# Optimization experiments

Measured on AMD Instinct MI355X. Metric: run time of the kernel, lower is better.

## Reference

```python
import jax, jax.numpy as jnp
import numpy as np

K = 8              # kernel_size
C_IN = 3           # input_channels
HID = 256          # hidden_state_size
MID = 256          # mid_layer_size
N_MAIN = 4         # num_main_layers
N_CLS = 1000       # num_classes
N_PIX = K * K      # num_pixel_values
IN_VEC = 2 + 1 + N_PIX * C_IN + HID   # 451
OUT_VEC = 2 + 1 + HID                 # 259
B, H, W = 128, 256, 256


def _lin_init(k, fan_in, fan_out):
    kw, kb = jax.random.split(k)
    bound = 1.0 / np.sqrt(fan_in)
    w = jax.random.uniform(kw, (fan_in, fan_out), jnp.float32, -bound, bound)
    b = jax.random.uniform(kb, (fan_out,), jnp.float32, -bound, bound)
    return w, b


def setup_inputs() -> dict:
    key = jax.random.key(0)
    ks = jax.random.split(key, 16)
    image = jax.random.normal(ks[0], (B, C_IN, H, W), jnp.float32)
    locations = jax.random.uniform(ks[1], (B, 2), jnp.float32)
    scales = jax.random.uniform(ks[2], (B, 1), jnp.float32)
    hidden_state = jax.random.normal(ks[3], (B, HID), jnp.float32)
    w0, b0 = _lin_init(ks[4], IN_VEC, MID)
    rws, rbs = [], []
    for i in range(N_MAIN):
        w, b = _lin_init(jax.random.fold_in(ks[5], i), MID, MID)
        rws.append(w); rbs.append(b)
    rw = jnp.stack(rws); rb = jnp.stack(rbs)          # [4,MID,MID], [4,MID]
    wf, bf = _lin_init(ks[6], MID, OUT_VEC)
    cw0, cb0 = _lin_init(ks[7], HID, MID)
    crw, crb = _lin_init(ks[8], MID, MID)
    cw1, cb1 = _lin_init(ks[9], MID, N_CLS)
    return {"image": image, "locations": locations, "scales": scales,
            "hidden_state": hidden_state, "w0": w0, "b0": b0, "rw": rw,
            "rb": rb, "wf": wf, "bf": bf, "cw0": cw0, "cb0": cb0,
            "crw": crw, "crb": crb, "cw1": cw1, "cb1": cb1}


def fourier_interp_2d(image, sample_points):
    """Band-limited (NUDFT) interpolation of image at continuous points.
    image: [B,C,H,W]; sample_points: [B,N,2] in normalized [0,1) (ij order).
    Returns [B,N,C]."""
    Bsz, C, Hh, Ww = image.shape
    F = jnp.fft.fft2(image)                       # [B,C,H,W] complex
    fy = jnp.fft.fftfreq(Hh) * Hh                 # integer freqs [H]
    fx = jnp.fft.fftfreq(Ww) * Ww                 # integer freqs [W]
    y = sample_points[..., 0]                     # [B,N]
    x = sample_points[..., 1]
    two_pi_i = 2j * jnp.pi
    Ey = jnp.exp(two_pi_i * y[..., None] * fy)    # [B,N,H]
    Ex = jnp.exp(two_pi_i * x[..., None] * fx)    # [B,N,W]
    tmp = jnp.einsum('bchw,bnh->bcnw', F, Ey)     # dominant compute
    vals = jnp.einsum('bcnw,bnw->bcn', tmp, Ex).real / (Hh * Ww)
    return jnp.transpose(vals, (0, 2, 1))         # [B,N,C]


def reference(image, locations, scales, hidden_state,
              w0, b0, rw, rb, wf, bf, cw0, cb0, crw, crb, cw1, cb1):
    Bsz = image.shape[0]
    # base meshgrid: [K,K,2], ij indexing, values arange(K)/K
    g = jnp.arange(K, dtype=image.dtype) / K
    mesh = jnp.stack(jnp.meshgrid(g, g, indexing='ij'), axis=-1)  # [K,K,2]
    coords = mesh[None] - locations[:, None, None, :]             # [B,K,K,2]
    coords = coords * scales[:, None, None, :]
    coords = coords.reshape(Bsz, N_PIX, 2)
    pix = fourier_interp_2d(image, coords)                        # [B,N,C]
    pix = pix.reshape(Bsz, N_PIX * C_IN)
    inp = jnp.concatenate([locations, scales, pix, hidden_state], axis=-1)
    h = inp @ w0 + b0
    for i in range(N_MAIN):
        h = jax.nn.relu(h @ rw[i] + rb[i] + h)
    out = jnp.tanh(h @ wf + bf)                                   # [B,OUT_VEC]
    new_loc = locations + out[:, :2]
    new_scale = scales + out[:, 2:3]
    new_hidden = hidden_state + out[:, 3:]
    c = jax.nn.relu(new_hidden @ cw0 + cb0)
    c = jax.nn.relu(c @ crw + crb + c)
    preds = jax.nn.softmax(c @ cw1 + cb1, axis=-1)
    # concat all outputs: [B, 2+1+HID+N_CLS]
    return jnp.concatenate([new_loc, new_scale, new_hidden, preds], axis=-1)
```

## Files before the change

### kernel.cpp

```cpp
#include <hip/hip_runtime.h>
#include <math.h>

#define BB 128
#define OUTROW 1259

typedef float vf4 __attribute__((ext_vector_type(4)));

__device__ __forceinline__ void dirichlet_ab(float t, float& A, float& Bv) {
    float r = t - rintf(t);
    float s256 = sinpif(256.0f * r);
    Bv = s256 * (1.0f / 256.0f);
    if (fabsf(r) < 1e-6f) {
        A = 1.0f;
    } else {
        float sp = sinpif(r), cp = cospif(r);
        A = Bv * cp / sp;
    }
}

__global__ __launch_bounds__(256) void interp_kernel(
    const float* __restrict__ image, const float* __restrict__ loc,
    const float* __restrict__ scl, float* __restrict__ pix)
{
    __shared__ float U[256 * 16];
    __shared__ float V[16 * 260];
    __shared__ float T[16 * 260];

    int bid = blockIdx.x;
    int b = bid / 3, c = bid % 3;
    int tid = threadIdx.x;
    float l0 = loc[2 * b], l1 = loc[2 * b + 1], sc = scl[b];

    {
        int p = tid;
        float tp = (float)p * (1.0f / 256.0f);
        #pragma unroll
        for (int iy = 0; iy < 8; ++iy) {
            float A, Bv;
            float y = ((float)iy * 0.125f - l0) * sc;
            dirichlet_ab(y - tp, A, Bv);
            int w = iy >> 1, o = iy & 1;
            U[p * 16 + w * 4 + o] = A;
            U[p * 16 + w * 4 + 2 + o] = Bv;
            float x = ((float)iy * 0.125f - l1) * sc;
            dirichlet_ab(x - tp, A, Bv);
            V[iy * 260 + p] = A;
            V[(8 + iy) * 260 + p] = Bv;
        }
    }
    __syncthreads();

    int wave = tid >> 6, lane = tid & 63;
    const float* img = image + (size_t)(b * 3 + c) * 65536 + lane * 4;

    float aA0[4] = {0, 0, 0, 0}, aA1[4] = {0, 0, 0, 0};
    float aB0[4] = {0, 0, 0, 0}, aB1[4] = {0, 0, 0, 0};
    #pragma unroll 4
    for (int p = 0; p < 256; ++p) {
        vf4 v = __builtin_nontemporal_load((const vf4*)(img + p * 256));
        const float4 u = *(const float4*)(&U[p * 16 + wave * 4]);
        aA0[0] += u.x * v[0]; aA0[1] += u.x * v[1]; aA0[2] += u.x * v[2]; aA0[3] += u.x * v[3];
        aA1[0] += u.y * v[0]; aA1[1] += u.y * v[1]; aA1[2] += u.y * v[2]; aA1[3] += u.y * v[3];
        aB0[0] += u.z * v[0]; aB0[1] += u.z * v[1]; aB0[2] += u.z * v[2]; aB0[3] += u.z * v[3];
        aB1[0] += u.w * v[0]; aB1[1] += u.w * v[1]; aB1[2] += u.w * v[2]; aB1[3] += u.w * v[3];
    }
    int iy0 = wave * 2;
    int q0 = lane * 4;
    #pragma unroll
    for (int j = 0; j < 4; ++j) {
        T[iy0 * 260 + q0 + j]       = aA0[j];
        T[(iy0 + 1) * 260 + q0 + j] = aA1[j];
        T[(8 + iy0) * 260 + q0 + j]     = aB0[j];
        T[(8 + iy0 + 1) * 260 + q0 + j] = aB1[j];
    }
    __syncthreads();

    int n = tid >> 2, sub = tid & 3;
    int iy = n >> 3, ix = n & 7;
    float s = 0.f;
    #pragma unroll 8
    for (int i = 0; i < 64; ++i) {
        int q = sub + 4 * i;
        s += T[iy * 260 + q] * V[ix * 260 + q] - T[(8 + iy) * 260 + q] * V[(8 + ix) * 260 + q];
    }
    s += __shfl_xor(s, 1);
    s += __shfl_xor(s, 2);
    if (sub == 0) pix[(b * 64 + n) * 3 + c] = s;
}

__device__ __forceinline__ void gemv256(const float* __restrict__ W,
                                        const float* __restrict__ s_src,
                                        float* __restrict__ s_part,
                                        int sub, int j4)
{
    float4 wv[16];
    float hv[16];
    #pragma unroll
    for (int t = 0; t < 16; ++t)
        wv[t] = *(const float4*)(W + (size_t)(sub + 16 * t) * 256 + j4);
    #pragma unroll
    for (int t = 0; t < 16; ++t)
        hv[t] = s_src[sub + 16 * t];
    float4 a = {0.f, 0.f, 0.f, 0.f};
    #pragma unroll
    for (int t = 0; t < 16; ++t) {
        a.x += hv[t] * wv[t].x; a.y += hv[t] * wv[t].y;
        a.z += hv[t] * wv[t].z; a.w += hv[t] * wv[t].w;
    }
    *(float4*)(&s_part[sub * 256 + j4]) = a;
}

__global__ __launch_bounds__(1024, 1) void mlp_main(
    const float* __restrict__ loc, const float* __restrict__ scl,
    const float* __restrict__ hidden, const float* __restrict__ pix,
    const float* __restrict__ w0, const float* __restrict__ b0,
    const float* __restrict__ rw, const float* __restrict__ rb,
    const float* __restrict__ wf, const float* __restrict__ bf,
    const float* __restrict__ cw0, const float* __restrict__ cb0,
    const float* __restrict__ crw, const float* __restrict__ crb,
    float* __restrict__ c1buf, float* __restrict__ out)
{
    __shared__ float s_in[452];
    __shared__ float s_h[256];
    __shared__ float s_c[256];
    __shared__ float s_o[260];
    __shared__ float s_part[16 * 260];
    __shared__ float s_b0[256], s_rb[1024], s_bf[260], s_cb0[256], s_crb[256];

    int b = blockIdx.x, tid = threadIdx.x;
    int jg = tid & 63, sub = tid >> 6;
    int j4 = jg * 4;
    float* orow = out + (size_t)b * OUTROW;

    if (tid < 2) s_in[tid] = loc[2 * b + tid];
    if (tid == 2) s_in[2] = scl[b];
    if (tid >= 256 && tid < 448) s_in[3 + (tid - 256)] = pix[b * 192 + (tid - 256)];
    if (tid >= 512 && tid < 768) s_in[195 + (tid - 512)] = hidden[b * 256 + (tid - 512)];
    if (tid < 256) s_b0[tid] = b0[tid];
    s_rb[tid] = rb[tid];
    if (tid < 259) s_bf[tid] = bf[tid];
    if (tid >= 256 && tid < 512) s_cb0[tid - 256] = cb0[tid - 256];
    if (tid >= 512 && tid < 768) s_crb[tid - 512] = crb[tid - 512];
    __syncthreads();

    {
        float4 acc = {0.f, 0.f, 0.f, 0.f};
        {
            float4 wv[14]; float hv[14];
            #pragma unroll
            for (int t = 0; t < 14; ++t)
                wv[t] = *(const float4*)(w0 + (size_t)(sub + 16 * t) * 256 + j4);
            #pragma unroll
            for (int t = 0; t < 14; ++t) hv[t] = s_in[sub + 16 * t];
            #pragma unroll
            for (int t = 0; t < 14; ++t) {
                acc.x += hv[t] * wv[t].x; acc.y += hv[t] * wv[t].y;
                acc.z += hv[t] * wv[t].z; acc.w += hv[t] * wv[t].w;
            }
        }
        {
            float4 wv[14]; float hv[14];
            #pragma unroll
            for (int t = 0; t < 14; ++t)
                wv[t] = *(const float4*)(w0 + (size_t)(sub + 16 * (t + 14)) * 256 + j4);
            #pragma unroll
            for (int t = 0; t < 14; ++t) hv[t] = s_in[sub + 16 * (t + 14)];
            #pragma unroll
            for (int t = 0; t < 14; ++t) {
                acc.x += hv[t] * wv[t].x; acc.y += hv[t] * wv[t].y;
                acc.z += hv[t] * wv[t].z; acc.w += hv[t] * wv[t].w;
            }
        }
        if (sub < 3) {
            int k = 448 + sub;
            float hv = s_in[k];
            float4 w = *(const float4*)(w0 + (size_t)k * 256 + j4);
            acc.x += hv * w.x; acc.y += hv * w.y; acc.z += hv * w.z; acc.w += hv * w.w;
        }
        *(float4*)(&s_part[sub * 256 + j4]) = acc;
    }
    __syncthreads();
    if (tid < 256) {
        float a = s_b0[tid];
        #pragma unroll
        for (int s = 0; s < 16; ++s) a += s_part[s * 256 + tid];
        s_h[tid] = a;
    }
    __syncthreads();

    #pragma unroll 1
    for (int L = 0; L < 4; ++L) {
        gemv256(rw + (size_t)L * 65536, s_h, s_part, sub, j4);
        __syncthreads();
        if (tid < 256) {
            float v = s_rb[L * 256 + tid] + s_h[tid];
            #pragma unroll
            for (int s = 0; s < 16; ++s) v += s_part[s * 256 + tid];
            s_h[tid] = fmaxf(v, 0.f);
        }
        __syncthreads();
    }

    {
        float a0 = 0.f, a1 = 0.f, a2 = 0.f, a3 = 0.f, e = 0.f;
        #pragma unroll 8
        for (int t = 0; t < 16; ++t) {
            int k = sub + 16 * t;
            float hv = s_h[k];
            const float* w = wf + (size_t)k * 259 + j4;
            a0 += hv * w[0]; a1 += hv * w[1]; a2 += hv * w[2]; a3 += hv * w[3];
            if (jg < 3) e += hv * wf[(size_t)k * 259 + 256 + jg];
        }
        s_part[sub * 260 + j4 + 0] = a0;
        s_part[sub * 260 + j4 + 1] = a1;
        s_part[sub * 260 + j4 + 2] = a2;
        s_part[sub * 260 + j4 + 3] = a3;
        if (jg < 3) s_part[sub * 260 + 256 + jg] = e;
    }
    __syncthreads();
    if (tid < 259) {
        float a = s_bf[tid];
        #pragma unroll
        for (int s = 0; s < 16; ++s) a += s_part[s * 260 + tid];
        s_o[tid] = tanhf(a);
    }
    __syncthreads();

    if (tid < 256) {
        float nh = s_in[195 + tid] + s_o[3 + tid];
        orow[3 + tid] = nh;
        s_h[tid] = nh;
    }
    if (tid == 256) orow[0] = s_in[0] + s_o[0];
    if (tid == 257) orow[1] = s_in[1] + s_o[1];
    if (tid == 258) orow[2] = s_in[2] + s_o[2];
    __syncthreads();

    gemv256(cw0, s_h, s_part, sub, j4);
    __syncthreads();
    if (tid < 256) {
        float v = s_cb0[tid];
        #pragma unroll
        for (int s = 0; s < 16; ++s) v += s_part[s * 256 + tid];
        s_c[tid] = fmaxf(v, 0.f);
    }
    __syncthreads();

    gemv256(crw, s_c, s_part, sub, j4);
    __syncthreads();
    if (tid < 256) {
        float v = s_crb[tid] + s_c[tid];
        #pragma unroll
        for (int s = 0; s < 16; ++s) v += s_part[s * 256 + tid];
        c1buf[b * 256 + tid] = fmaxf(v, 0.f);
    }
}

__global__ __launch_bounds__(1024, 1) void logits_kernel(
    const float* __restrict__ c1buf, const float* __restrict__ cw1,
    const float* __restrict__ cb1, float* __restrict__ logits)
{
    __shared__ float s_c1[256];
    __shared__ float s_part[32 * 128];

    int b = blockIdx.x, s = blockIdx.y, tid = threadIdx.x;
    if (tid < 256) s_c1[tid] = c1buf[b * 256 + tid];
    __syncthreads();

    int cg = tid & 31, sub = tid >> 5;
    int c4 = cg * 4;
    int col0 = s * 128 + c4;
    bool valid = (col0 + 3) < 1000;

    float4 acc = {0.f, 0.f, 0.f, 0.f};
    if (valid) {
        float4 wv[8]; float hv[8];
        #pragma unroll
        for (int t = 0; t < 8; ++t)
            wv[t] = *(const float4*)(cw1 + (size_t)(sub + 32 * t) * 1000 + col0);
        #pragma unroll
        for (int t = 0; t < 8; ++t) hv[t] = s_c1[sub + 32 * t];
        #pragma unroll
        for (int t = 0; t < 8; ++t) {
            acc.x += hv[t] * wv[t].x; acc.y += hv[t] * wv[t].y;
            acc.z += hv[t] * wv[t].z; acc.w += hv[t] * wv[t].w;
        }
    }
    *(float4*)(&s_part[sub * 128 + c4]) = acc;
    __syncthreads();

    if (tid < 128) {
        int col = s * 128 + tid;
        if (col < 1000) {
            float a = cb1[col];
            #pragma unroll
            for (int ss = 0; ss < 32; ++ss) a += s_part[ss * 128 + tid];
            logits[(size_t)b * 1000 + col] = a;
        }
    }
}

__global__ __launch_bounds__(1024) void softmax_kernel(
    const float* __restrict__ logits, float* __restrict__ out)
{
    __shared__ float s_red[32];
    int b = blockIdx.x, tid = threadIdx.x;
    float* orow = out + (size_t)b * OUTROW;

    float lgv = (tid < 1000) ? logits[(size_t)b * 1000 + tid] : -1e30f;

    int lane = tid & 63, wid = tid >> 6;
    float m = lgv;
    #pragma unroll
    for (int off = 1; off < 64; off <<= 1) m = fmaxf(m, __shfl_xor(m, off));
    if (lane == 0) s_red[wid] = m;
    __syncthreads();
    m = s_red[0];
    #pragma unroll
    for (int w = 1; w < 16; ++w) m = fmaxf(m, s_red[w]);

    float e = (tid < 1000) ? expf(lgv - m) : 0.f;
    float lsum = e;
    #pragma unroll
    for (int off = 1; off < 64; off <<= 1) lsum += __shfl_xor(lsum, off);
    if (lane == 0) s_red[16 + wid] = lsum;
    __syncthreads();
    float total = 0.f;
    #pragma unroll
    for (int w = 0; w < 16; ++w) total += s_red[16 + w];

    if (tid < 1000) orow[259 + tid] = e / total;
}

extern "C" void kernel_launch(void* const* d_in, const int* in_sizes, int n_in,
                              void* d_out, int out_size, void* d_ws, size_t ws_size,
                              hipStream_t stream) {
    const float* image  = (const float*)d_in[0];
    const float* loc    = (const float*)d_in[1];
    const float* scl    = (const float*)d_in[2];
    const float* hidden = (const float*)d_in[3];
    const float* w0  = (const float*)d_in[4];
    const float* b0  = (const float*)d_in[5];
    const float* rw  = (const float*)d_in[6];
    const float* rb  = (const float*)d_in[7];
    const float* wf  = (const float*)d_in[8];
    const float* bf  = (const float*)d_in[9];
    const float* cw0 = (const float*)d_in[10];
    const float* cb0 = (const float*)d_in[11];
    const float* crw = (const float*)d_in[12];
    const float* crb = (const float*)d_in[13];
    const float* cw1 = (const float*)d_in[14];
    const float* cb1 = (const float*)d_in[15];

    float* ws     = (float*)d_ws;
    float* pix    = ws;
    float* c1buf  = ws + 24576;
    float* logits = ws + 24576 + 32768;

    hipLaunchKernelGGL(interp_kernel, dim3(BB * 3), dim3(256), 0, stream,
                       image, loc, scl, pix);
    hipLaunchKernelGGL(mlp_main, dim3(BB), dim3(1024), 0, stream,
                       loc, scl, hidden, pix,
                       w0, b0, rw, rb, wf, bf, cw0, cb0, crw, crb,
                       c1buf, (float*)d_out);
    hipLaunchKernelGGL(logits_kernel, dim3(BB, 8), dim3(1024), 0, stream,
                       c1buf, cw1, cb1, logits);
    hipLaunchKernelGGL(softmax_kernel, dim3(BB), dim3(1024), 0, stream,
                       logits, (float*)d_out);
}
```

Before: 85.52 us.

## Convert MLP weights to bf16 in interp kernel and read bf16 in GEMVs

Adds 2048 extra blocks to the interpolation kernel that convert every MLP and classifier weight matrix to bf16 in a workspace buffer, padding wf rows to 260. The GEMV kernels then load ushort4 instead of float4 and widen to fp32 before the FMA. The aim is to halve weight traffic in mlp_main and logits_kernel, which re-read the weights for every batch row. The cost is an extra full read and write of all weights on every call, plus reduced weight precision.

Result: slower. 87.78 us (+2.6%).

```diff
diff --git a/kernel.cpp b/kernel.cpp
--- a/kernel.cpp
+++ b/kernel.cpp
@@ -5,6 +5,31 @@
 #define OUTROW 1259
 
 typedef float vf4 __attribute__((ext_vector_type(4)));
+
+__device__ __forceinline__ ushort f2b(float x) {
+    unsigned u = __float_as_uint(x);
+    unsigned r = (u + 0x7FFFu + ((u >> 16) & 1u)) >> 16;
+    return (ushort)r;
+}
+__device__ __forceinline__ float b2f(ushort b) {
+    return __uint_as_float(((unsigned)b) << 16);
+}
+__device__ __forceinline__ float4 bf4tof(ushort4 u) {
+    float4 f;
+    f.x = __uint_as_float((unsigned)u.x << 16);
+    f.y = __uint_as_float((unsigned)u.y << 16);
+    f.z = __uint_as_float((unsigned)u.z << 16);
+    f.w = __uint_as_float((unsigned)u.w << 16);
+    return f;
+}
+
+#define OFF_W0   0u
+#define OFF_RW   115456u
+#define OFF_CW0  377600u
+#define OFF_CRW  443136u
+#define OFF_CW1  508672u
+#define OFF_WF   764672u
+#define N_CONV   831232u
 
 __device__ __forceinline__ void dirichlet_ab(float t, float& A, float& Bv) {
     float r = t - rintf(t);
@@ -18,17 +43,44 @@
     }
 }
 
-__global__ __launch_bounds__(256) void interp_kernel(
+__global__ __launch_bounds__(256) void interp_convert_kernel(
     const float* __restrict__ image, const float* __restrict__ loc,
-    const float* __restrict__ scl, float* __restrict__ pix)
+    const float* __restrict__ scl, float* __restrict__ pix,
+    const float* __restrict__ w0, const float* __restrict__ rw,
+    const float* __restrict__ wf, const float* __restrict__ cw0,
+    const float* __restrict__ crw, const float* __restrict__ cw1,
+    ushort* __restrict__ bfa)
 {
     __shared__ float U[256 * 16];
     __shared__ float V[16 * 260];
     __shared__ float T[16 * 260];
 
     int bid = blockIdx.x;
+    int tid = threadIdx.x;
+
+    if (bid >= 384) {
+        unsigned g = (unsigned)(bid - 384) * 256u + (unsigned)tid;
+        for (unsigned i = g; i < N_CONV; i += 2048u * 256u) {
+            unsigned j = i; float v;
+            if (j < 115456u) { v = w0[j]; bfa[OFF_W0 + j] = f2b(v); continue; }
+            j -= 115456u;
+            if (j < 262144u) { v = rw[j]; bfa[OFF_RW + j] = f2b(v); continue; }
+            j -= 262144u;
+            if (j < 65536u) { v = cw0[j]; bfa[OFF_CW0 + j] = f2b(v); continue; }
+            j -= 65536u;
+            if (j < 65536u) { v = crw[j]; bfa[OFF_CRW + j] = f2b(v); continue; }
+            j -= 65536u;
+            if (j < 256000u) { v = cw1[j]; bfa[OFF_CW1 + j] = f2b(v); continue; }
+            j -= 256000u;
+            {
+                unsigned k = j / 260u, c = j - k * 260u;
+                bfa[OFF_WF + j] = (c < 259u) ? f2b(wf[k * 259u + c]) : (ushort)0;
+            }
+        }
+        return;
+    }
+
     int b = bid / 3, c = bid % 3;
-    int tid = threadIdx.x;
     float l0 = loc[2 * b], l1 = loc[2 * b + 1], sc = scl[b];
 
     {
@@ -88,24 +140,25 @@
     if (sub == 0) pix[(b * 64 + n) * 3 + c] = s;
 }
 
-__device__ __forceinline__ void gemv256(const float* __restrict__ W,
-                                        const float* __restrict__ s_src,
-                                        float* __restrict__ s_part,
-                                        int sub, int j4)
+__device__ __forceinline__ void gemv256b(const ushort* __restrict__ W,
+                                         const float* __restrict__ s_src,
+                                         float* __restrict__ s_part,
+                                         int sub, int j4)
 {
-    float4 wv[16];
+    ushort4 wv[16];
     float hv[16];
     #pragma unroll
     for (int t = 0; t < 16; ++t)
-        wv[t] = *(const float4*)(W + (size_t)(sub + 16 * t) * 256 + j4);
+        wv[t] = *(const ushort4*)(W + (size_t)(sub + 16 * t) * 256 + j4);
     #pragma unroll
     for (int t = 0; t < 16; ++t)
         hv[t] = s_src[sub + 16 * t];
     float4 a = {0.f, 0.f, 0.f, 0.f};
     #pragma unroll
     for (int t = 0; t < 16; ++t) {
-        a.x += hv[t] * wv[t].x; a.y += hv[t] * wv[t].y;
-        a.z += hv[t] * wv[t].z; a.w += hv[t] * wv[t].w;
+        float4 w = bf4tof(wv[t]);
+        a.x += hv[t] * w.x; a.y += hv[t] * w.y;
+        a.z += hv[t] * w.z; a.w += hv[t] * w.w;
     }
     *(float4*)(&s_part[sub * 256 + j4]) = a;
 }
@@ -113,11 +166,10 @@
 __global__ __launch_bounds__(1024, 1) void mlp_main(
     const float* __restrict__ loc, const float* __restrict__ scl,
     const float* __restrict__ hidden, const float* __restrict__ pix,
-    const float* __restrict__ w0, const float* __restrict__ b0,
-    const float* __restrict__ rw, const float* __restrict__ rb,
-    const float* __restrict__ wf, const float* __restrict__ bf,
-    const float* __restrict__ cw0, const float* __restrict__ cb0,
-    const float* __restrict__ crw, const float* __restrict__ crb,
+    const ushort* __restrict__ bfa,
+    const float* __restrict__ b0, const float* __restrict__ rb,
+    const float* __restrict__ bf, const float* __restrict__ cb0,
+    const float* __restrict__ crb,
     float* __restrict__ c1buf, float* __restrict__ out)
 {
     __shared__ float s_in[452];
@@ -126,6 +178,12 @@
     __shared__ float s_o[260];
     __shared__ float s_part[16 * 260];
     __shared__ float s_b0[256], s_rb[1024], s_bf[260], s_cb0[256], s_crb[256];
+
+    const ushort* w0b  = bfa + OFF_W0;
+    const ushort* rwb  = bfa + OFF_RW;
+    const ushort* wfb  = bfa + OFF_WF;
+    const ushort* cw0b = bfa + OFF_CW0;
+    const ushort* crwb = bfa + OFF_CRW;
 
     int b = blockIdx.x, tid = threadIdx.x;
     int jg = tid & 63, sub = tid >> 6;
@@ -146,35 +204,37 @@
     {
         float4 acc = {0.f, 0.f, 0.f, 0.f};
         {
-            float4 wv[14]; float hv[14];
+            ushort4 wv[14]; float hv[14];
             #pragma unroll
             for (int t = 0; t < 14; ++t)
-                wv[t] = *(const float4*)(w0 + (size_t)(sub + 16 * t) * 256 + j4);
+                wv[t] = *(const ushort4*)(w0b + (size_t)(sub + 16 * t) * 256 + j4);
             #pragma unroll
             for (int t = 0; t < 14; ++t) hv[t] = s_in[sub + 16 * t];
             #pragma unroll
             for (int t = 0; t < 14; ++t) {
-                acc.x += hv[t] * wv[t].x; acc.y += hv[t] * wv[t].y;
-                acc.z += hv[t] * wv[t].z; acc.w += hv[t] * wv[t].w;
+                float4 w = bf4tof(wv[t]);
+                acc.x += hv[t] * w.x; acc.y += hv[t] * w.y;
+                acc.z += hv[t] * w.z; acc.w += hv[t] * w.w;
             }
         }
         {
-            float4 wv[14]; float hv[14];
+            ushort4 wv[14]; float hv[14];
             #pragma unroll
             for (int t = 0; t < 14; ++t)
-                wv[t] = *(const float4*)(w0 + (size_t)(sub + 16 * (t + 14)) * 256 + j4);
+                wv[t] = *(const ushort4*)(w0b + (size_t)(sub + 16 * (t + 14)) * 256 + j4);
             #pragma unroll
             for (int t = 0; t < 14; ++t) hv[t] = s_in[sub + 16 * (t + 14)];
             #pragma unroll
             for (int t = 0; t < 14; ++t) {
-                acc.x += hv[t] * wv[t].x; acc.y += hv[t] * wv[t].y;
-                acc.z += hv[t] * wv[t].z; acc.w += hv[t] * wv[t].w;
+                float4 w = bf4tof(wv[t]);
+                acc.x += hv[t] * w.x; acc.y += hv[t] * w.y;
+                acc.z += hv[t] * w.z; acc.w += hv[t] * w.w;
             }
         }
         if (sub < 3) {
             int k = 448 + sub;
             float hv = s_in[k];
-            float4 w = *(const float4*)(w0 + (size_t)k * 256 + j4);
+            float4 w = bf4tof(*(const ushort4*)(w0b + (size_t)k * 256 + j4));
             acc.x += hv * w.x; acc.y += hv * w.y; acc.z += hv * w.z; acc.w += hv * w.w;
         }
         *(float4*)(&s_part[sub * 256 + j4]) = acc;
@@ -190,7 +250,7 @@
 
     #pragma unroll 1
     for (int L = 0; L < 4; ++L) {
-        gemv256(rw + (size_t)L * 65536, s_h, s_part, sub, j4);
+        gemv256b(rwb + (size_t)L * 65536, s_h, s_part, sub, j4);
         __syncthreads();
         if (tid < 256) {
             float v = s_rb[L * 256 + tid] + s_h[tid];
@@ -203,13 +263,20 @@
 
     {
         float a0 = 0.f, a1 = 0.f, a2 = 0.f, a3 = 0.f, e = 0.f;
-        #pragma unroll 8
+        ushort4 wv[16]; float hv[16]; ushort ev[16];
+        #pragma unroll
         for (int t = 0; t < 16; ++t) {
             int k = sub + 16 * t;
-            float hv = s_h[k];
-            const float* w = wf + (size_t)k * 259 + j4;
-            a0 += hv * w[0]; a1 += hv * w[1]; a2 += hv * w[2]; a3 += hv * w[3];
-            if (jg < 3) e += hv * wf[(size_t)k * 259 + 256 + jg];
+            wv[t] = *(const ushort4*)(wfb + (size_t)k * 260 + j4);
+            if (jg < 3) ev[t] = wfb[(size_t)k * 260 + 256 + jg];
+        }
+        #pragma unroll
+        for (int t = 0; t < 16; ++t) hv[t] = s_h[sub + 16 * t];
+        #pragma unroll
+        for (int t = 0; t < 16; ++t) {
+            float4 w = bf4tof(wv[t]);
+            a0 += hv[t] * w.x; a1 += hv[t] * w.y; a2 += hv[t] * w.z; a3 += hv[t] * w.w;
+            if (jg < 3) e += hv[t] * b2f(ev[t]);
         }
         s_part[sub * 260 + j4 + 0] = a0;
         s_part[sub * 260 + j4 + 1] = a1;
@@ -236,7 +303,7 @@
     if (tid == 258) orow[2] = s_in[2] + s_o[2];
     __syncthreads();
 
-    gemv256(cw0, s_h, s_part, sub, j4);
+    gemv256b(cw0b, s_h, s_part, sub, j4);
     __syncthreads();
     if (tid < 256) {
         float v = s_cb0[tid];
@@ -246,7 +313,7 @@
     }
     __syncthreads();
 
-    gemv256(crw, s_c, s_part, sub, j4);
+    gemv256b(crwb, s_c, s_part, sub, j4);
     __syncthreads();
     if (tid < 256) {
         float v = s_crb[tid] + s_c[tid];
@@ -257,12 +324,14 @@
 }
 
 __global__ __launch_bounds__(1024, 1) void logits_kernel(
-    const float* __restrict__ c1buf, const float* __restrict__ cw1,
+    const float* __restrict__ c1buf, const ushort* __restrict__ bfa,
     const float* __restrict__ cb1, float* __restrict__ logits)
 {
     __shared__ float s_c1[256];
     __shared__ float s_part[32 * 128];
 
+    const ushort* cw1b = bfa + OFF_CW1;
+
     int b = blockIdx.x, s = blockIdx.y, tid = threadIdx.x;
     if (tid < 256) s_c1[tid] = c1buf[b * 256 + tid];
     __syncthreads();
@@ -274,16 +343,17 @@
 
     float4 acc = {0.f, 0.f, 0.f, 0.f};
     if (valid) {
-        float4 wv[8]; float hv[8];
+        ushort4 wv[8]; float hv[8];
         #pragma unroll
         for (int t = 0; t < 8; ++t)
-            wv[t] = *(const float4*)(cw1 + (size_t)(sub + 32 * t) * 1000 + col0);
+            wv[t] = *(const ushort4*)(cw1b + (size_t)(sub + 32 * t) * 1000 + col0);
         #pragma unroll
         for (int t = 0; t < 8; ++t) hv[t] = s_c1[sub + 32 * t];
         #pragma unroll
         for (int t = 0; t < 8; ++t) {
-            acc.x += hv[t] * wv[t].x; acc.y += hv[t] * wv[t].y;
-            acc.z += hv[t] * wv[t].z; acc.w += hv[t] * wv[t].w;
+            float4 w = bf4tof(wv[t]);
+            acc.x += hv[t] * w.x; acc.y += hv[t] * w.y;
+            acc.z += hv[t] * w.z; acc.w += hv[t] * w.w;
         }
     }
     *(float4*)(&s_part[sub * 128 + c4]) = acc;
@@ -356,15 +426,15 @@
     float* pix    = ws;
     float* c1buf  = ws + 24576;
     float* logits = ws + 24576 + 32768;
-
-    hipLaunchKernelGGL(interp_kernel, dim3(BB * 3), dim3(256), 0, stream,
-                       image, loc, scl, pix);
+    ushort* bfa   = (ushort*)(ws + 185344);
+
+    hipLaunchKernelGGL(interp_convert_kernel, dim3(384 + 2048), dim3(256), 0, stream,
+                       image, loc, scl, pix, w0, rw, wf, cw0, crw, cw1, bfa);
     hipLaunchKernelGGL(mlp_main, dim3(BB), dim3(1024), 0, stream,
-                       loc, scl, hidden, pix,
-                       w0, b0, rw, rb, wf, bf, cw0, cb0, crw, crb,
-                       c1buf, (float*)d_out);
+                       loc, scl, hidden, pix, bfa,
+                       b0, rb, bf, cb0, crb, c1buf, (float*)d_out);
     hipLaunchKernelGGL(logits_kernel, dim3(BB, 8), dim3(1024), 0, stream,
-                       c1buf, cw1, cb1, logits);
+                       c1buf, bfa, cb1, logits);
     hipLaunchKernelGGL(softmax_kernel, dim3(BB), dim3(1024), 0, stream,
                        logits, (float*)d_out);
 }
```
